# Kernel optimization log

Hardware: AMD Instinct MI355X
Metric: run time of the kernel (lower is better)

Reference implementation:

```python
import jax, jax.numpy as jnp
import numpy as np

B, T, N, D, H, S, L, O = 32, 12, 2048, 2, 64, 2, 2, 1


def setup_inputs() -> dict:
    key = jax.random.key(0)
    ks = jax.random.split(key, 32)
    inp = {}
    inp["x"] = jax.random.normal(ks[0], (B, T, N, D), dtype=jnp.float32)
    sup = jax.random.uniform(ks[1], (S, N, N), dtype=jnp.float32)
    # row-normalized, like random-walk diffusion transition matrices
    inp["supports"] = sup / jnp.sum(sup, axis=-1, keepdims=True)
    i = 2
    for l in range(L):
        din = (D if l == 0 else H) + H  # concat([x, h]) width
        for g in ("r", "u", "c"):
            inp[f"W{g}{l}"] = jax.random.normal(ks[i], (din, H), dtype=jnp.float32) * 0.02; i += 1
            inp[f"b{g}{l}"] = jnp.zeros((H,), jnp.float32)
        inp[f"Wd{l}"] = jax.random.normal(ks[i], (S, H, H), dtype=jnp.float32) * 0.02; i += 1
        inp[f"bd{l}"] = jnp.zeros((S, H), jnp.float32)
    inp["Wo"] = jax.random.normal(ks[i], (H, O), dtype=jnp.float32) * 0.02
    inp["bo"] = jnp.zeros((O,), jnp.float32)
    return inp


def _cell(x_t, h, supports, Wr, br, Wu, bu, Wc, bc, Wd, bd):
    # x_t: [B,N,din-H], h: [B,N,H]
    xh = jnp.concatenate([x_t, h], axis=-1)
    r = jax.nn.sigmoid(xh @ Wr + br)  # computed but unused, as in the source module
    u = jax.nn.sigmoid(xh @ Wu + bu)
    c = jnp.tanh(xh @ Wc + bc)
    # Diffusion conv is DEAD CODE in the source (h_diff never used); kept for fidelity,
    # DCE'd under jit. snm,bmh,shk -> per-support graph matmul + linear, summed.
    h_diff = h + jnp.einsum('snm,bmh,shk->bnk', supports, h, Wd) + jnp.sum(bd, axis=0)
    del r, h_diff
    return u * h + (1.0 - u) * c


def reference(x, supports,
              Wr0, br0, Wu0, bu0, Wc0, bc0, Wd0, bd0,
              Wr1, br1, Wu1, bu1, Wc1, bc1, Wd1, bd1,
              Wo, bo):
    p0 = (Wr0, br0, Wu0, bu0, Wc0, bc0, Wd0, bd0)
    p1 = (Wr1, br1, Wu1, bu1, Wc1, bc1, Wd1, bd1)

    def step(carry, x_t):
        h0, h1 = carry
        h0 = _cell(x_t, h0, supports, *p0)
        h1 = _cell(h0, h1, supports, *p1)  # dropout p=0.0 -> identity
        return (h0, h1), None

    h_init = (jnp.zeros((B, N, H), x.dtype), jnp.zeros((B, N, H), x.dtype))
    (h0, h1), _ = jax.lax.scan(step, h_init, jnp.swapaxes(x, 0, 1))  # scan over T
    return h1 @ Wo + bo  # [B, N, O]
```

## Files before the change

kernel.cpp:

```cpp
#include <hip/hip_runtime.h>


#define TSTEPS 12

__device__ __forceinline__ float fsig(float z) {
    z = fminf(fmaxf(z, -30.f), 30.f);
    return 1.f / (1.f + __expf(-z));
}
__device__ __forceinline__ float ftanh(float z) {
    z = fminf(fmaxf(z, -15.f), 15.f);
    float e = __expf(2.f * z);
    return 1.f - 2.f / (e + 1.f);
}


__global__ void pack_weights(const float* __restrict__ Wu0, const float* __restrict__ bu0,
                             const float* __restrict__ Wc0, const float* __restrict__ bc0,
                             const float* __restrict__ Wu1, const float* __restrict__ bu1,
                             const float* __restrict__ Wc1, const float* __restrict__ bc1,
                             const float* __restrict__ Wo, const float* __restrict__ bo,
                             float* __restrict__ Wp) {
    const int tid = blockIdx.x * blockDim.x + threadIdx.x;
    const int nthr = gridDim.x * blockDim.x;
    for (int i = tid; i < 8192; i += nthr) {
        const int k = i >> 7, r = i & 127, wv = r >> 4, j = r & 15;
        const int col = wv * 8 + (j & 7);
        Wp[i] = (j < 8) ? Wu0[(2 + k) * 64 + col] : Wc0[(2 + k) * 64 + col];
    }
    for (int i = tid; i < 256; i += nthr) {
        const int k = i >> 7, r = i & 127, wv = r >> 4, j = r & 15;
        const int col = wv * 8 + (j & 7);
        Wp[8192 + i] = (j < 8) ? Wu0[k * 64 + col] : Wc0[k * 64 + col];
    }
    for (int i = tid; i < 16384; i += nthr) {
        const int k = i >> 7, r = i & 127, wv = r >> 4, j = r & 15;
        const int col = wv * 8 + (j & 7);
        Wp[8448 + i] = (j < 8) ? Wu1[k * 64 + col] : Wc1[k * 64 + col];
    }
    for (int i = tid; i < 128; i += nthr) {
        const int wv = i >> 4, j = i & 15;
        const int col = wv * 8 + (j & 7);
        Wp[24832 + i] = (j < 8) ? bu0[col] : bc0[col];
        Wp[24960 + i] = (j < 8) ? bu1[col] : bc1[col];
    }
    for (int i = tid; i < 64; i += nthr) Wp[25088 + i] = Wo[i];
    if (tid == 0) Wp[25152] = bo[0];
}

#define REP8(X) X(0) X(1) X(2) X(3) X(4) X(5) X(6) X(7)

#define INITJ(J) zu##J##0 = bp_[J]; zu##J##1 = bp_[J]; \
                 zc##J##0 = bp_[8 + J]; zc##J##1 = bp_[8 + J];

#define FMAJ(J) \
    zu##J##0 = __builtin_fmaf(hv.x, wk_[J], zu##J##0); \
    zu##J##1 = __builtin_fmaf(hv.y, wk_[J], zu##J##1); \
    zc##J##0 = __builtin_fmaf(hv.x, wk_[8 + J], zc##J##0); \
    zc##J##1 = __builtin_fmaf(hv.y, wk_[8 + J], zc##J##1);

#define KSTEP(WB, KK) { \
    const float2 hv = *(const float2*)(Aptr + (size_t)(KK) * 128); \
    const float* wk_ = (WB) + (size_t)(KK) * 128; \
    REP8(FMAJ) }

#define XPJ(J) \
    zu##J##0 = __builtin_fmaf(xv.x, wx_[J], __builtin_fmaf(xv.y, wx_[128 + J], zu##J##0)); \
    zu##J##1 = __builtin_fmaf(xv.z, wx_[J], __builtin_fmaf(xv.w, wx_[128 + J], zu##J##1)); \
    zc##J##0 = __builtin_fmaf(xv.x, wx_[8 + J], __builtin_fmaf(xv.y, wx_[136 + J], zc##J##0)); \
    zc##J##1 = __builtin_fmaf(xv.z, wx_[8 + J], __builtin_fmaf(xv.w, wx_[136 + J], zc##J##1));

#define ACTJ(J) { \
    const float2 ho = *(const float2*)(hb_ + (J) * 128); \
    float u_, c_; \
    u_ = fsig(zu##J##0); c_ = ftanh(zc##J##0); \
    zu##J##0 = __builtin_fmaf(u_, ho.x, (1.f - u_) * c_); \
    u_ = fsig(zu##J##1); c_ = ftanh(zc##J##1); \
    zu##J##1 = __builtin_fmaf(u_, ho.y, (1.f - u_) * c_); }

#define STJ(J) *(float2*)(hb_ + (J) * 128) = make_float2(zu##J##0, zu##J##1);

#define POJ(J) part0 = __builtin_fmaf(zu##J##0, wo_[J], part0); \
               part1 = __builtin_fmaf(zu##J##1, wo_[J], part1);

__global__ __launch_bounds__(512, 4) void dcrnn_main(const float* __restrict__ x,
                                                     const float* __restrict__ Wp,
                                                     float* __restrict__ out) {
    __shared__ float A[128 * 128];
    __shared__ float P[8 * 128];

    const int tid = threadIdx.x;
    const int lane = tid & 63;
    const int w = __builtin_amdgcn_readfirstlane(tid >> 6);

    const int s0 = blockIdx.x * 128;
    const int b = s0 >> 11;
    const int n0 = s0 & 2047;

    const float* W0w = Wp + w * 16;
    const float* Wxw = Wp + 8192 + w * 16;
    const float* W1w = Wp + 8448 + w * 16;
    const float* B0w = Wp + 24832 + w * 16;
    const float* B1w = Wp + 24960 + w * 16;

    for (int i = tid; i < 128 * 128; i += 512) A[i] = 0.f;
    __syncthreads();

    const float* Aptr0 = A + 2 * lane;
    float* hb0 = A + (size_t)(w * 8) * 128 + 2 * lane;
    float* hb1 = A + (size_t)(64 + w * 8) * 128 + 2 * lane;

    const float* xlane = x + (size_t)(b * TSTEPS) * 4096 + (size_t)(n0 + 2 * lane) * 2;

    float zu00, zu01, zu10, zu11, zu20, zu21, zu30, zu31;
    float zu40, zu41, zu50, zu51, zu60, zu61, zu70, zu71;
    float zc00, zc01, zc10, zc11, zc20, zc21, zc30, zc31;
    float zc40, zc41, zc50, zc51, zc60, zc61, zc70, zc71;

#pragma unroll 1
    for (int t = 0; t < TSTEPS; ++t) {
        const float4 xv = *(const float4*)(xlane + (size_t)t * 4096);

        { const float* bp_ = B0w; REP8(INITJ) }
        {
            const float* Aptr = Aptr0;
#pragma unroll 1
            for (int k = 0; k < 64; k += 4) {
                KSTEP(W0w, k + 0)
                KSTEP(W0w, k + 1)
                KSTEP(W0w, k + 2)
                KSTEP(W0w, k + 3)
            }
        }
        { const float* wx_ = Wxw; REP8(XPJ) }
        { const float* hb_ = hb0; REP8(ACTJ) }
        __syncthreads();
        { float* hb_ = hb0; REP8(STJ) }
        __syncthreads();

        { const float* bp_ = B1w; REP8(INITJ) }
        {
            const float* Aptr = Aptr0;
#pragma unroll 1
            for (int k = 0; k < 128; k += 4) {
                KSTEP(W1w, k + 0)
                KSTEP(W1w, k + 1)
                KSTEP(W1w, k + 2)
                KSTEP(W1w, k + 3)
            }
        }
        { const float* hb_ = hb1; REP8(ACTJ) }
        __syncthreads();
        { float* hb_ = hb1; REP8(STJ) }
    }

    float part0 = 0.f, part1 = 0.f;
    { const float* wo_ = Wp + 25088 + w * 8; REP8(POJ) }
    *(float2*)&P[w * 128 + 2 * lane] = make_float2(part0, part1);
    __syncthreads();
    if (tid < 128) {
        float acc = Wp[25152];
#pragma unroll
        for (int wv = 0; wv < 8; ++wv) acc += P[wv * 128 + tid];
        out[s0 + tid] = acc;
    }
}

extern "C" void kernel_launch(void* const* d_in, const int* in_sizes, int n_in,
                              void* d_out, int out_size, void* d_ws, size_t ws_size,
                              hipStream_t stream) {
    const float* x   = (const float*)d_in[0];
    const float* Wu0 = (const float*)d_in[4];
    const float* bu0 = (const float*)d_in[5];
    const float* Wc0 = (const float*)d_in[6];
    const float* bc0 = (const float*)d_in[7];
    const float* Wu1 = (const float*)d_in[12];
    const float* bu1 = (const float*)d_in[13];
    const float* Wc1 = (const float*)d_in[14];
    const float* bc1 = (const float*)d_in[15];
    const float* Wo  = (const float*)d_in[18];
    const float* bo  = (const float*)d_in[19];

    float* Wp = (float*)d_ws;

    hipLaunchKernelGGL(pack_weights, dim3(64), dim3(256), 0, stream,
                       Wu0, bu0, Wc0, bc0, Wu1, bu1, Wc1, bc1, Wo, bo, Wp);
    hipLaunchKernelGGL(dcrnn_main, dim3(65536 / 128), dim3(512), 0, stream,
                       x, Wp, (float*)d_out);
}
```

Baseline: 589.1 us.

## Software-pipeline recurrent GEMM with double-buffered float4 weight and hidden-state prefetch

The inner recurrent matvec loops are restructured into a two-stage register pipeline. Weights are loaded as float4 vectors into A/B register sets and hidden-state pairs are prefetched from shared memory one stage ahead of the FMAs. The input projection is folded into the same compute macro. The wave index is no longer made uniform with readfirstlane, so weight loads likely become per-lane vector loads instead of scalar loads. The extra 64 weight registers risk spilling under the 512x4 launch bounds.

```diff
diff --git a/kernel.cpp b/kernel.cpp
--- a/kernel.cpp
+++ b/kernel.cpp
@@ -47,40 +47,41 @@
     if (tid == 0) Wp[25152] = bo[0];
 }
 
+#define F(a, b, c) __builtin_fmaf((a), (b), (c))
 #define REP8(X) X(0) X(1) X(2) X(3) X(4) X(5) X(6) X(7)
 
 #define INITJ(J) zu##J##0 = bp_[J]; zu##J##1 = bp_[J]; \
                  zc##J##0 = bp_[8 + J]; zc##J##1 = bp_[8 + J];
 
-#define FMAJ(J) \
-    zu##J##0 = __builtin_fmaf(hv.x, wk_[J], zu##J##0); \
-    zu##J##1 = __builtin_fmaf(hv.y, wk_[J], zu##J##1); \
-    zc##J##0 = __builtin_fmaf(hv.x, wk_[8 + J], zc##J##0); \
-    zc##J##1 = __builtin_fmaf(hv.y, wk_[8 + J], zc##J##1);
+#define KCOMP(HV, P0, P1, P2, P3) \
+  zu00=F(HV.x,P0.x,zu00); zu01=F(HV.y,P0.x,zu01); zc00=F(HV.x,P2.x,zc00); zc01=F(HV.y,P2.x,zc01); \
+  zu10=F(HV.x,P0.y,zu10); zu11=F(HV.y,P0.y,zu11); zc10=F(HV.x,P2.y,zc10); zc11=F(HV.y,P2.y,zc11); \
+  zu20=F(HV.x,P0.z,zu20); zu21=F(HV.y,P0.z,zu21); zc20=F(HV.x,P2.z,zc20); zc21=F(HV.y,P2.z,zc21); \
+  zu30=F(HV.x,P0.w,zu30); zu31=F(HV.y,P0.w,zu31); zc30=F(HV.x,P2.w,zc30); zc31=F(HV.y,P2.w,zc31); \
+  zu40=F(HV.x,P1.x,zu40); zu41=F(HV.y,P1.x,zu41); zc40=F(HV.x,P3.x,zc40); zc41=F(HV.y,P3.x,zc41); \
+  zu50=F(HV.x,P1.y,zu50); zu51=F(HV.y,P1.y,zu51); zc50=F(HV.x,P3.y,zc50); zc51=F(HV.y,P3.y,zc51); \
+  zu60=F(HV.x,P1.z,zu60); zu61=F(HV.y,P1.z,zu61); zc60=F(HV.x,P3.z,zc60); zc61=F(HV.y,P3.z,zc61); \
+  zu70=F(HV.x,P1.w,zu70); zu71=F(HV.y,P1.w,zu71); zc70=F(HV.x,P3.w,zc70); zc71=F(HV.y,P3.w,zc71);
 
-#define KSTEP(WB, KK) { \
-    const float2 hv = *(const float2*)(Aptr + (size_t)(KK) * 128); \
-    const float* wk_ = (WB) + (size_t)(KK) * 128; \
-    REP8(FMAJ) }
+#define LOADW(N, BASE, KK) { \
+    const float4* q_ = (BASE) + (size_t)(KK) * 32; \
+    w##N##0 = q_[0];  w##N##1 = q_[1];  w##N##2 = q_[2];  w##N##3 = q_[3]; \
+    w##N##4 = q_[32]; w##N##5 = q_[33]; w##N##6 = q_[34]; w##N##7 = q_[35]; }
 
-#define XPJ(J) \
-    zu##J##0 = __builtin_fmaf(xv.x, wx_[J], __builtin_fmaf(xv.y, wx_[128 + J], zu##J##0)); \
-    zu##J##1 = __builtin_fmaf(xv.z, wx_[J], __builtin_fmaf(xv.w, wx_[128 + J], zu##J##1)); \
-    zc##J##0 = __builtin_fmaf(xv.x, wx_[8 + J], __builtin_fmaf(xv.y, wx_[136 + J], zc##J##0)); \
-    zc##J##1 = __builtin_fmaf(xv.z, wx_[8 + J], __builtin_fmaf(xv.w, wx_[136 + J], zc##J##1));
+#define LDH(HV, KK) HV = *(const float2*)(Aptr + (size_t)(KK) * 128);
 
 #define ACTJ(J) { \
     const float2 ho = *(const float2*)(hb_ + (J) * 128); \
     float u_, c_; \
     u_ = fsig(zu##J##0); c_ = ftanh(zc##J##0); \
-    zu##J##0 = __builtin_fmaf(u_, ho.x, (1.f - u_) * c_); \
+    zu##J##0 = F(u_, ho.x, (1.f - u_) * c_); \
     u_ = fsig(zu##J##1); c_ = ftanh(zc##J##1); \
-    zu##J##1 = __builtin_fmaf(u_, ho.y, (1.f - u_) * c_); }
+    zu##J##1 = F(u_, ho.y, (1.f - u_) * c_); }
 
 #define STJ(J) *(float2*)(hb_ + (J) * 128) = make_float2(zu##J##0, zu##J##1);
 
-#define POJ(J) part0 = __builtin_fmaf(zu##J##0, wo_[J], part0); \
-               part1 = __builtin_fmaf(zu##J##1, wo_[J], part1);
+#define POJ(J) part0 = F(zu##J##0, wo_[J], part0); \
+               part1 = F(zu##J##1, wo_[J], part1);
 
 __global__ __launch_bounds__(512, 4) void dcrnn_main(const float* __restrict__ x,
                                                      const float* __restrict__ Wp,
@@ -90,22 +91,22 @@
 
     const int tid = threadIdx.x;
     const int lane = tid & 63;
-    const int w = __builtin_amdgcn_readfirstlane(tid >> 6);
+    const int w = tid >> 6;
 
     const int s0 = blockIdx.x * 128;
     const int b = s0 >> 11;
     const int n0 = s0 & 2047;
 
-    const float* W0w = Wp + w * 16;
-    const float* Wxw = Wp + 8192 + w * 16;
-    const float* W1w = Wp + 8448 + w * 16;
+    const float4* Wq0 = (const float4*)Wp + w * 4;
+    const float4* Wqx = (const float4*)(Wp + 8192) + w * 4;
+    const float4* Wq1 = (const float4*)(Wp + 8448) + w * 4;
     const float* B0w = Wp + 24832 + w * 16;
     const float* B1w = Wp + 24960 + w * 16;
 
     for (int i = tid; i < 128 * 128; i += 512) A[i] = 0.f;
     __syncthreads();
 
-    const float* Aptr0 = A + 2 * lane;
+    const float* Aptr = A + 2 * lane;
     float* hb0 = A + (size_t)(w * 8) * 128 + 2 * lane;
     float* hb1 = A + (size_t)(64 + w * 8) * 128 + 2 * lane;
 
@@ -115,38 +116,47 @@
     float zu40, zu41, zu50, zu51, zu60, zu61, zu70, zu71;
     float zc00, zc01, zc10, zc11, zc20, zc21, zc30, zc31;
     float zc40, zc41, zc50, zc51, zc60, zc61, zc70, zc71;
+    float4 wA0, wA1, wA2, wA3, wA4, wA5, wA6, wA7;
+    float4 wB0, wB1, wB2, wB3, wB4, wB5, wB6, wB7;
+    float2 hA0, hA1, hB0, hB1;
 
 #pragma unroll 1
     for (int t = 0; t < TSTEPS; ++t) {
         const float4 xv = *(const float4*)(xlane + (size_t)t * 4096);
 
         { const float* bp_ = B0w; REP8(INITJ) }
+        LOADW(A, Wq0, 0) LDH(hA0, 0) LDH(hA1, 1)
+#pragma unroll 1
+        for (int k = 0; k < 64; k += 4) {
+            LOADW(B, Wq0, k + 2) LDH(hB0, k + 2) LDH(hB1, k + 3)
+            KCOMP(hA0, wA0, wA1, wA2, wA3)
+            KCOMP(hA1, wA4, wA5, wA6, wA7)
+            LOADW(A, Wq0, k + 4) LDH(hA0, k + 4) LDH(hA1, k + 5)
+            KCOMP(hB0, wB0, wB1, wB2, wB3)
+            KCOMP(hB1, wB4, wB5, wB6, wB7)
+        }
         {
-            const float* Aptr = Aptr0;
-#pragma unroll 1
-            for (int k = 0; k < 64; k += 4) {
-                KSTEP(W0w, k + 0)
-                KSTEP(W0w, k + 1)
-                KSTEP(W0w, k + 2)
-                KSTEP(W0w, k + 3)
-            }
+            LOADW(A, Wqx, 0)
+            const float2 xa_ = make_float2(xv.x, xv.z);
+            const float2 xb_ = make_float2(xv.y, xv.w);
+            KCOMP(xa_, wA0, wA1, wA2, wA3)
+            KCOMP(xb_, wA4, wA5, wA6, wA7)
         }
-        { const float* wx_ = Wxw; REP8(XPJ) }
         { const float* hb_ = hb0; REP8(ACTJ) }
         __syncthreads();
         { float* hb_ = hb0; REP8(STJ) }
         __syncthreads();
 
         { const float* bp_ = B1w; REP8(INITJ) }
-        {
-            const float* Aptr = Aptr0;
+        LOADW(A, Wq1, 0) LDH(hA0, 0) LDH(hA1, 1)
 #pragma unroll 1
-            for (int k = 0; k < 128; k += 4) {
-                KSTEP(W1w, k + 0)
-                KSTEP(W1w, k + 1)
-                KSTEP(W1w, k + 2)
-                KSTEP(W1w, k + 3)
-            }
+        for (int k = 0; k < 128; k += 4) {
+            LOADW(B, Wq1, k + 2) LDH(hB0, k + 2) LDH(hB1, k + 3)
+            KCOMP(hA0, wA0, wA1, wA2, wA3)
+            KCOMP(hA1, wA4, wA5, wA6, wA7)
+            LOADW(A, Wq1, k + 4) LDH(hA0, k + 4) LDH(hA1, k + 5)
+            KCOMP(hB0, wB0, wB1, wB2, wB3)
+            KCOMP(hB1, wB4, wB5, wB6, wB7)
         }
         { const float* hb_ = hb1; REP8(ACTJ) }
         __syncthreads();
```

After: 1.285 ms. +118.1%, slower.
